# Kernel optimization log

Measured on AMD Instinct MI355X. Metric: run time of the kernel, lower is better.

## Reference

```python
import jax, jax.numpy as jnp
import numpy as np
import math

HID = 2048
NH = 8
KVH = 1
HD = 256
REP = NH // KVH
THETA = 10000.0
B, S = 2, 2048
NEG = -1e9  # additive mask value for disallowed positions


def setup_inputs() -> dict:
    key = jax.random.key(0)
    ks = jax.random.split(key, 6)
    x = jax.random.normal(ks[0], (B, S, HID), dtype=jnp.float32)
    # causal additive mask [B,1,S,S]
    causal = jnp.tril(jnp.ones((S, S), dtype=bool))
    attn_mask = jnp.where(causal, 0.0, NEG).astype(jnp.float32)[None, None]
    attn_mask = jnp.broadcast_to(attn_mask, (B, 1, S, S))
    pos_ids = jnp.broadcast_to(jnp.arange(S, dtype=jnp.int64 if jax.config.jax_enable_x64 else jnp.int32), (B, S))
    sc = 0.02
    wq = jax.random.normal(ks[1], (HID, NH * HD), dtype=jnp.float32) * sc
    wk = jax.random.normal(ks[2], (HID, KVH * HD), dtype=jnp.float32) * sc
    wv = jax.random.normal(ks[3], (HID, KVH * HD), dtype=jnp.float32) * sc
    wo = jax.random.normal(ks[4], (NH * HD, HID), dtype=jnp.float32) * sc
    return {"x": x, "attn_mask": attn_mask, "pos_ids": pos_ids,
            "wq": wq, "wk": wk, "wv": wv, "wo": wo}


def _rotate_half(t):
    h = t.shape[-1] // 2
    return jnp.concatenate([-t[..., h:], t[..., :h]], axis=-1)


def _rope_cos_sin(pos_ids, dtype):
    inv_freq = 1.0 / (THETA ** (jnp.arange(0, HD, 2, dtype=jnp.float32) / HD))  # [HD/2]
    freqs = pos_ids.astype(jnp.float32)[:, :, None] * inv_freq[None, None, :]  # [B,S,HD/2]
    emb = jnp.concatenate([freqs, freqs], axis=-1)                              # [B,S,HD]
    # unsqueeze head dim -> [B,1,S,HD]
    return jnp.cos(emb)[:, None].astype(dtype), jnp.sin(emb)[:, None].astype(dtype)


def reference(x, attn_mask, pos_ids, wq, wk, wv, wo):
    b, s, _ = x.shape
    q = (x @ wq).reshape(b, s, NH, HD).transpose(0, 2, 1, 3)    # [B,NH,S,HD]
    k = (x @ wk).reshape(b, s, KVH, HD).transpose(0, 2, 1, 3)   # [B,KVH,S,HD]
    v = (x @ wv).reshape(b, s, KVH, HD).transpose(0, 2, 1, 3)   # [B,KVH,S,HD]
    cos, sin = _rope_cos_sin(pos_ids, q.dtype)
    q = q * cos + _rotate_half(q) * sin
    k = k * cos + _rotate_half(k) * sin
    # GQA: group query heads over shared KV head instead of materializing repeat_kv
    qg = q.reshape(b, KVH, REP, s, HD)
    scores = jnp.einsum('bgrqd,bgkd->bgrqk', qg, k) / math.sqrt(HD)  # [B,KVH,REP,S,S]
    scores = scores.reshape(b, NH, s, s) + attn_mask
    attn = jax.nn.softmax(scores.astype(jnp.float32), axis=-1).astype(q.dtype)  # [B,NH,S,S]
    # dropout p=0.0 -> identity
    pg = attn.reshape(b, KVH, REP, s, s)
    out = jnp.einsum('bgrqk,bgkd->bgrqd', pg, v).reshape(b, NH, s, HD)
    out = out.transpose(0, 2, 1, 3).reshape(b, s, NH * HD) @ wo  # [B,S,HID]
    return out, attn
```

## Files before the change

### kernel.cpp

```cpp
#include <hip/hip_runtime.h>
#include <cstdint>
#include <cmath>

#define HID_ 2048
#define NH_ 8
#define HD_ 256
#define B_ 2
#define S_ 2048
#define BS_ (B_*S_)
#define QKVW_ 2560

typedef short short8 __attribute__((ext_vector_type(8)));
typedef float floatx4 __attribute__((ext_vector_type(4)));

static __device__ __forceinline__ unsigned short f2bf(float f) {
  union { float f; unsigned u; } v; v.f = f;
  return (unsigned short)((v.u + 0x7FFFu + ((v.u >> 16) & 1u)) >> 16);
}
static __device__ __forceinline__ float bf2f(unsigned short h) {
  union { unsigned u; float f; } v; v.u = ((unsigned)h) << 16;
  return v.f;
}

static __device__ __forceinline__ void gload_lds16(const void* g, void* l) {
  __builtin_amdgcn_global_load_lds(
      (const __attribute__((address_space(1))) unsigned int*)g,
      (__attribute__((address_space(3))) unsigned int*)l, 16, 0, 0);
}


__global__ void cast_f32_bf16_k(const float* __restrict__ in, unsigned short* __restrict__ out, long n) {
  long i = ((long)blockIdx.x * blockDim.x + threadIdx.x) * 4;
  if (i >= n) return;
  float4 v = *reinterpret_cast<const float4*>(in + i);
  ushort4 o; o.x = f2bf(v.x); o.y = f2bf(v.y); o.z = f2bf(v.z); o.w = f2bf(v.w);
  *reinterpret_cast<ushort4*>(out + i) = o;
}

__global__ void transpose_f2b_k(const float* __restrict__ in, unsigned short* __restrict__ out, int R, int C) {
  __shared__ float tile[32][33];
  int c0 = blockIdx.x * 32, r0 = blockIdx.y * 32;
  int tx = threadIdx.x, ty = threadIdx.y;
  #pragma unroll
  for (int i = 0; i < 4; i++)
    tile[ty + i*8][tx] = in[(long)(r0 + ty + i*8) * C + c0 + tx];
  __syncthreads();
  #pragma unroll
  for (int i = 0; i < 4; i++)
    out[(long)(c0 + ty + i*8) * R + r0 + tx] = f2bf(tile[tx][ty + i*8]);
}

__global__ void transpose_strided_k(const unsigned short* __restrict__ in, unsigned short* __restrict__ out,
                                    int ld_in, int ld_out, long in_bs, long out_bs) {
  __shared__ unsigned short tile[32][33];
  in += (long)blockIdx.z * in_bs; out += (long)blockIdx.z * out_bs;
  int c0 = blockIdx.x * 32, r0 = blockIdx.y * 32;
  int tx = threadIdx.x, ty = threadIdx.y;
  #pragma unroll
  for (int i = 0; i < 4; i++)
    tile[ty + i*8][tx] = in[(long)(r0 + ty + i*8) * ld_in + c0 + tx];
  __syncthreads();
  #pragma unroll
  for (int i = 0; i < 4; i++)
    out[(long)(c0 + ty + i*8) * ld_out + r0 + tx] = tile[tx][ty + i*8];
}

__global__ void rope_k(unsigned short* __restrict__ qk, const int* __restrict__ pos_ids,
                       int heads, int row_stride, long total) {
  long idx = (long)blockIdx.x * blockDim.x + threadIdx.x;
  if (idx >= total) return;
  int per_row = heads * (HD_/2);
  int r  = (int)(idx / per_row);
  int rem = (int)(idx % per_row);
  int h = rem / (HD_/2);
  int i = rem % (HD_/2);
  float posf = (float)pos_ids[r];
  float freq = expf(-(float)i * (logf(10000.0f) / 128.0f));
  float ang = posf * freq;
  float c = cosf(ang), s = sinf(ang);
  unsigned short* p = qk + (long)r * row_stride + (long)h * HD_;
  float a = bf2f(p[i]), b = bf2f(p[i + 128]);
  p[i]       = f2bf(a * c - b * s);
  p[i + 128] = f2bf(b * c + a * s);
}

template<int EPI>
__global__ __launch_bounds__(256)
void gemm_bt_k(const void* __restrict__ Av, const unsigned short* __restrict__ Bt,
               void* __restrict__ Cv, int K, long lda, long ldb, long ldc) {
  __shared__ unsigned short Al[128 * 32];
  __shared__ unsigned short Bl[128 * 32];

  int tid = threadIdx.x;
  int lane = tid & 63, wave = tid >> 6;
  int bm = blockIdx.y * 128, bn = blockIdx.x * 128;

  const unsigned short* Abase = (const unsigned short*)Av + (long)bm * lda;
  const unsigned short* Bbase = Bt + (long)bn * ldb;

  floatx4 zero = {0.f, 0.f, 0.f, 0.f};
  floatx4 acc[4][4];
  #pragma unroll
  for (int i = 0; i < 4; i++)
    #pragma unroll
    for (int j = 0; j < 4; j++) acc[i][j] = zero;

  const int wm = (wave >> 1) * 64, wn = (wave & 1) * 64;
  const int lr = lane & 15, lq = lane >> 4;

  for (int k0 = 0; k0 < K; k0 += 32) {
    #pragma unroll
    for (int c = 0; c < 2; c++) {
      int e = c * 2048 + tid * 8;
      int row = e >> 5, col = e & 31;
      gload_lds16(Abase + (long)row * lda + k0 + col, (char*)Al + c * 4096 + wave * 1024);
    }
    #pragma unroll
    for (int c = 0; c < 2; c++) {
      int e = c * 2048 + tid * 8;
      int row = e >> 5, col = e & 31;
      gload_lds16(Bbase + (long)row * ldb + k0 + col, (char*)Bl + c * 4096 + wave * 1024);
    }
    __syncthreads();

    short8 af[4], bfr[4];
    #pragma unroll
    for (int i = 0; i < 4; i++)
      af[i] = *reinterpret_cast<const short8*>(&Al[(wm + i*16 + lr) * 32 + lq * 8]);
    #pragma unroll
    for (int j = 0; j < 4; j++)
      bfr[j] = *reinterpret_cast<const short8*>(&Bl[(wn + j*16 + lr) * 32 + lq * 8]);
    #pragma unroll
    for (int i = 0; i < 4; i++)
      #pragma unroll
      for (int j = 0; j < 4; j++)
        acc[i][j] = __builtin_amdgcn_mfma_f32_16x16x32_bf16(af[i], bfr[j], acc[i][j], 0, 0, 0);
    __syncthreads();
  }

  if (EPI == 0) {
    unsigned short* C = (unsigned short*)Cv;
    #pragma unroll
    for (int i = 0; i < 4; i++)
      #pragma unroll
      for (int r = 0; r < 4; r++) {
        int row = bm + wm + i*16 + lq*4 + r;
        #pragma unroll
        for (int j = 0; j < 4; j++) {
          int col = bn + wn + j*16 + lr;
          C[(long)row * ldc + col] = f2bf(acc[i][j][r]);
        }
      }
  } else {
    float* C = (float*)Cv;
    #pragma unroll
    for (int i = 0; i < 4; i++)
      #pragma unroll
      for (int r = 0; r < 4; r++) {
        int row = bm + wm + i*16 + lq*4 + r;
        #pragma unroll
        for (int j = 0; j < 4; j++) {
          int col = bn + wn + j*16 + lr;
          C[(long)row * ldc + col] = acc[i][j][r];
        }
      }
  }
}

__global__ __launch_bounds__(256, 2)
void attn_fused_k(const unsigned short* __restrict__ qkv, const unsigned short* __restrict__ v_t,
                  float* __restrict__ attn, unsigned short* __restrict__ o_bf,
                  float* __restrict__ rowinv) {
  int z = blockIdx.x;
  int b = z >> 3, h = z & 7;
  int t = 31 - blockIdx.y;
  int bm = t * 64;
  int nkt = t / 2 + 1;

  const unsigned short* Qg = qkv + (long)b * S_ * QKVW_ + (long)h * HD_;
  const unsigned short* Kg = qkv + (long)b * S_ * QKVW_ + 2048;
  const unsigned short* Vt = v_t + (long)b * HD_ * S_;
  float* Az = attn + (long)z * S_ * S_;

  __shared__ unsigned short Ql[64 * 256];
  __shared__ unsigned short KPl[128 * 64];
  __shared__ unsigned short Vl[128 * 64];

  int tid = threadIdx.x;
  int lane = tid & 63, wave = tid >> 6;
  int lr = lane & 15, lq = lane >> 4;
  int lx = lr & 7;

  {
    int ce = nkt * 128;
    int perrow = (S_ - ce) >> 2;
    float4 zf = {0.f, 0.f, 0.f, 0.f};
    for (int i = tid; i < 64 * perrow; i += 256) {
      int r = i / perrow, c = i - r * perrow;
      *reinterpret_cast<float4*>(Az + (long)(bm + r) * S_ + ce + c * 4) = zf;
    }
  }

  #pragma unroll
  for (int c = 0; c < 8; c++) {
    int q = c * 256 + tid;
    int row = q >> 5, g = q & 31;
    gload_lds16(Qg + (long)(bm + row) * QKVW_ + ((g ^ (row & 7)) << 3),
                (char*)Ql + c * 4096 + wave * 1024);
  }

  floatx4 zero = {0.f, 0.f, 0.f, 0.f};
  floatx4 oacc[16];
  #pragma unroll
  for (int j = 0; j < 16; j++) oacc[j] = zero;
  float rsum[4] = {0.f, 0.f, 0.f, 0.f};

  for (int kt = 0; kt < nkt; kt++) {
    floatx4 sacc[8];
    #pragma unroll
    for (int j = 0; j < 8; j++) sacc[j] = zero;

    #pragma unroll
    for (int k0 = 0; k0 < HD_; k0 += 64) {
      #pragma unroll
      for (int c = 0; c < 4; c++) {
        int q = c * 256 + tid;
        int row = q >> 3, g = q & 7;
        gload_lds16(Kg + (long)(kt * 128 + row) * QKVW_ + k0 + ((g ^ (row & 7)) << 3),
                    (char*)KPl + c * 4096 + wave * 1024);
      }
      __syncthreads();
      #pragma unroll
      for (int kk = 0; kk < 2; kk++) {
        int gq = (k0 >> 3) + kk * 4 + lq;
        short8 aq = *reinterpret_cast<const short8*>(&Ql[(wave*16 + lr) * 256 + ((gq ^ lx) << 3)]);
        #pragma unroll
        for (int j = 0; j < 8; j++) {
          short8 bk = *reinterpret_cast<const short8*>(&KPl[(j*16 + lr) * 64 + (((kk*4 + lq) ^ lx) << 3)]);
          sacc[j] = __builtin_amdgcn_mfma_f32_16x16x32_bf16(aq, bk, sacc[j], 0, 0, 0);
        }
      }
      __syncthreads();
    }

    #pragma unroll
    for (int j = 0; j < 8; j++)
      #pragma unroll
      for (int r = 0; r < 4; r++) {
        int row_l = wave*16 + lq*4 + r;
        int col_g = kt*128 + j*16 + lr;
        float p = (col_g <= bm + row_l) ? __expf(sacc[j][r] * 0.0625f) : 0.f;
        Az[(long)(bm + row_l) * S_ + col_g] = p;
        KPl[row_l * 128 + ((j*16 + lr) ^ ((row_l & 7) << 3))] = f2bf(p);
        rsum[r] += p;
      }

    #pragma unroll
    for (int ch = 0; ch < 2; ch++) {
      short8 ap[2];
      #pragma unroll
      for (int kk = 0; kk < 2; kk++)
        ap[kk] = *reinterpret_cast<const short8*>(
            &KPl[(wave*16 + lr) * 128 + ((ch*64 + kk*32 + lq*8) ^ (lx << 3))]);
      #pragma unroll
      for (int dh = 0; dh < 2; dh++) {
        #pragma unroll
        for (int c = 0; c < 4; c++) {
          int q = c * 256 + tid;
          int row = q >> 3, g = q & 7;
          gload_lds16(Vt + (long)(dh*128 + row) * S_ + kt*128 + ch*64 + ((g ^ (row & 7)) << 3),
                      (char*)Vl + c * 4096 + wave * 1024);
        }
        __syncthreads();
        #pragma unroll
        for (int kk = 0; kk < 2; kk++) {
          #pragma unroll
          for (int j2 = 0; j2 < 8; j2++) {
            short8 bv = *reinterpret_cast<const short8*>(
                &Vl[(j2*16 + lr) * 64 + (((kk*4 + lq) ^ lx) << 3)]);
            oacc[dh*8 + j2] = __builtin_amdgcn_mfma_f32_16x16x32_bf16(ap[kk], bv, oacc[dh*8 + j2], 0, 0, 0);
          }
        }
        __syncthreads();
      }
    }
  }

  #pragma unroll
  for (int r = 0; r < 4; r++) {
    float s = rsum[r];
    #pragma unroll
    for (int o = 1; o < 16; o <<= 1) s += __shfl_xor(s, o, 64);
    rsum[r] = 1.0f / s;
  }
  if (lr == 0) {
    #pragma unroll
    for (int r = 0; r < 4; r++)
      rowinv[(long)z * S_ + bm + wave*16 + lq*4 + r] = rsum[r];
  }

  unsigned short* C = o_bf + (long)b * S_ * HID_ + (long)h * HD_;
  #pragma unroll
  for (int dh = 0; dh < 2; dh++)
    #pragma unroll
    for (int j2 = 0; j2 < 8; j2++)
      #pragma unroll
      for (int r = 0; r < 4; r++) {
        int row = bm + wave*16 + lq*4 + r;
        int col = dh*128 + j2*16 + lr;
        C[(long)row * HID_ + col] = f2bf(oacc[dh*8 + j2][r] * rsum[r]);
      }
}

__global__ __launch_bounds__(256)
void attn_rescale_k(float* __restrict__ attn, const float* __restrict__ rowinv) {
  int z = blockIdx.y;
  int i = blockIdx.x;
  int m = (int)((sqrtf(8.f * (float)i + 1.f) - 1.f) * 0.5f);
  while ((m + 1) * (m + 2) / 2 <= i) m++;
  while (m * (m + 1) / 2 > i) m--;
  int n = i - m * (m + 1) / 2;

  int tid = threadIdx.x;
  int rr = tid >> 5, cc = tid & 31;
  float* base = attn + (long)z * S_ * S_ + (long)(m * 128) * S_ + n * 128;
  const float* invb = rowinv + (long)z * S_ + m * 128;
  #pragma unroll 4
  for (int it = 0; it < 16; it++) {
    int row = it * 8 + rr;
    float inv = invb[row];
    float4* p = reinterpret_cast<float4*>(base + (long)row * S_) + cc;
    float4 v = *p;
    v.x *= inv; v.y *= inv; v.z *= inv; v.w *= inv;
    *p = v;
  }
}


extern "C" void kernel_launch(void* const* d_in, const int* in_sizes, int n_in,
                              void* d_out, int out_size, void* d_ws, size_t ws_size,
                              hipStream_t stream) {
  (void)in_sizes; (void)n_in; (void)out_size; (void)ws_size;
  const float* x   = (const float*)d_in[0];
  const int*   pos = (const int*)d_in[2];
  const float* wq  = (const float*)d_in[3];
  const float* wk  = (const float*)d_in[4];
  const float* wv  = (const float*)d_in[5];
  const float* wo  = (const float*)d_in[6];
  float* out  = (float*)d_out;
  float* attn = out + (long)B_ * S_ * HID_;

  char* p = (char*)d_ws;
  auto take = [&](size_t n) { char* r = p; p += (n + 255) & ~(size_t)255; return r; };
  unsigned short* x_bf   = (unsigned short*)take((size_t)BS_ * HID_ * 2);
  unsigned short* wqkv_t = (unsigned short*)take((size_t)QKVW_ * HID_ * 2);
  unsigned short* wo_t   = (unsigned short*)take((size_t)HID_ * HID_ * 2);
  unsigned short* qkv    = (unsigned short*)take((size_t)BS_ * QKVW_ * 2);
  unsigned short* v_t    = (unsigned short*)take((size_t)B_ * HD_ * S_ * 2);
  unsigned short* o_bf   = (unsigned short*)take((size_t)BS_ * HID_ * 2);
  float*          rinv   = (float*)take((size_t)B_ * NH_ * S_ * 4);

  dim3 tb(32, 8);

  cast_f32_bf16_k<<<(BS_ * HID_) / 1024, 256, 0, stream>>>(x, x_bf, (long)BS_ * HID_);

  transpose_f2b_k<<<dim3(HID_/32, HID_/32), tb, 0, stream>>>(wq, wqkv_t, HID_, HID_);
  transpose_f2b_k<<<dim3(HD_/32,  HID_/32), tb, 0, stream>>>(wk, wqkv_t + (size_t)2048 * HID_, HID_, HD_);
  transpose_f2b_k<<<dim3(HD_/32,  HID_/32), tb, 0, stream>>>(wv, wqkv_t + (size_t)2304 * HID_, HID_, HD_);
  transpose_f2b_k<<<dim3(HID_/32, HID_/32), tb, 0, stream>>>(wo, wo_t, HID_, HID_);

  gemm_bt_k<0><<<dim3(QKVW_/128, BS_/128), 256, 0, stream>>>(
      x_bf, wqkv_t, qkv, HID_, HID_, HID_, QKVW_);

  rope_k<<<(BS_ * NH_ * (HD_/2)) / 256, 256, 0, stream>>>(
      qkv, pos, NH_, QKVW_, (long)BS_ * NH_ * (HD_/2));
  rope_k<<<(BS_ * (HD_/2)) / 256, 256, 0, stream>>>(
      qkv + 2048, pos, 1, QKVW_, (long)BS_ * (HD_/2));

  transpose_strided_k<<<dim3(HD_/32, S_/32, B_), tb, 0, stream>>>(
      qkv + 2304, v_t, QKVW_, S_, (long)S_ * QKVW_, (long)HD_ * S_);

  attn_fused_k<<<dim3(B_ * NH_, S_/64), 256, 0, stream>>>(qkv, v_t, attn, o_bf, rinv);

  attn_rescale_k<<<dim3(136, B_ * NH_), 256, 0, stream>>>(attn, rinv);

  gemm_bt_k<1><<<dim3(HID_/128, BS_/128), 256, 0, stream>>>(
      o_bf, wo_t, out, HID_, HID_, HID_, HID_);
}
```

Measured before the change: 694.1 us.

## Double-buffer K/V tiles in LDS and keep Q fragments in registers

Restructures the fused attention loop to double-buffer K and V tiles in shared memory, issuing the next chunk's async loads before computing on the current one so each stage needs only one barrier instead of two. Q is loaded once into registers instead of LDS, which frees shared memory. Attention-probability stores are paired through a lane shuffle into float2 writes. This adds register pressure from the 8 Q fragments and more complex buffer-index logic, and reuses a K buffer to hold P.

```diff
diff --git a/kernel.cpp b/kernel.cpp
--- a/kernel.cpp
+++ b/kernel.cpp
@@ -182,14 +182,12 @@
   const unsigned short* Vt = v_t + (long)b * HD_ * S_;
   float* Az = attn + (long)z * S_ * S_;
 
-  __shared__ unsigned short Ql[64 * 256];
-  __shared__ unsigned short KPl[128 * 64];
-  __shared__ unsigned short Vl[128 * 64];
+  __shared__ unsigned short Kb[2][128 * 64];
+  __shared__ unsigned short Vb[2][128 * 64];
 
   int tid = threadIdx.x;
   int lane = tid & 63, wave = tid >> 6;
   int lr = lane & 15, lq = lane >> 4;
-  int lx = lr & 7;
 
   {
     int ce = nkt * 128;
@@ -201,13 +199,37 @@
     }
   }
 
-  #pragma unroll
-  for (int c = 0; c < 8; c++) {
-    int q = c * 256 + tid;
-    int row = q >> 5, g = q & 31;
-    gload_lds16(Qg + (long)(bm + row) * QKVW_ + ((g ^ (row & 7)) << 3),
-                (char*)Ql + c * 4096 + wave * 1024);
-  }
+  short8 aq[8];
+  {
+    const unsigned short* qrow = Qg + (long)(bm + wave*16 + lr) * QKVW_;
+    #pragma unroll
+    for (int f = 0; f < 8; f++)
+      aq[f] = *reinterpret_cast<const short8*>(qrow + f*32 + lq*8);
+  }
+
+  auto stageK = [&](int kt_, int c_) {
+    char* dst = (char*)Kb[(kt_ + c_) & 1];
+    const unsigned short* src = Kg + (long)(kt_ * 128) * QKVW_ + c_ * 64;
+    #pragma unroll
+    for (int cc = 0; cc < 4; cc++) {
+      int q = cc * 256 + tid;
+      int row = q >> 3, g = q & 7;
+      gload_lds16(src + (long)row * QKVW_ + ((g ^ (row & 7)) << 3),
+                  dst + cc * 4096 + wave * 1024);
+    }
+  };
+  auto stageV = [&](int kt_, int p_) {
+    int dh = p_ & 1, sh = p_ >> 1;
+    char* dst = (char*)Vb[p_ & 1];
+    const unsigned short* src = Vt + (long)(dh * 128) * S_ + kt_ * 128 + sh * 64;
+    #pragma unroll
+    for (int cc = 0; cc < 4; cc++) {
+      int q = cc * 256 + tid;
+      int row = q >> 3, g = q & 7;
+      gload_lds16(src + (long)row * S_ + ((g ^ (row & 7)) << 3),
+                  dst + cc * 4096 + wave * 1024);
+    }
+  };
 
   floatx4 zero = {0.f, 0.f, 0.f, 0.f};
   floatx4 oacc[16];
@@ -215,74 +237,91 @@
   for (int j = 0; j < 16; j++) oacc[j] = zero;
   float rsum[4] = {0.f, 0.f, 0.f, 0.f};
 
+  stageK(0, 0);
+  __syncthreads();
+
   for (int kt = 0; kt < nkt; kt++) {
+    int pb = kt & 1;
     floatx4 sacc[8];
     #pragma unroll
     for (int j = 0; j < 8; j++) sacc[j] = zero;
 
     #pragma unroll
-    for (int k0 = 0; k0 < HD_; k0 += 64) {
-      #pragma unroll
-      for (int c = 0; c < 4; c++) {
-        int q = c * 256 + tid;
-        int row = q >> 3, g = q & 7;
-        gload_lds16(Kg + (long)(kt * 128 + row) * QKVW_ + k0 + ((g ^ (row & 7)) << 3),
-                    (char*)KPl + c * 4096 + wave * 1024);
+    for (int c = 0; c < 4; c++) {
+      if (c < 3) stageK(kt, c + 1);
+      if (c == 2) stageV(kt, 0);
+      if (c == 3) stageV(kt, 1);
+      const unsigned short* Kc = Kb[(kt + c) & 1];
+      #pragma unroll
+      for (int kk = 0; kk < 2; kk++) {
+        #pragma unroll
+        for (int j = 0; j < 8; j++) {
+          int R = j*16 + lr, G = kk*4 + lq;
+          short8 bk = *reinterpret_cast<const short8*>(&Kc[R*64 + ((G ^ (R & 7)) << 3)]);
+          sacc[j] = __builtin_amdgcn_mfma_f32_16x16x32_bf16(aq[c*2 + kk], bk, sacc[j], 0, 0, 0);
+        }
       }
       __syncthreads();
-      #pragma unroll
-      for (int kk = 0; kk < 2; kk++) {
-        int gq = (k0 >> 3) + kk * 4 + lq;
-        short8 aq = *reinterpret_cast<const short8*>(&Ql[(wave*16 + lr) * 256 + ((gq ^ lx) << 3)]);
-        #pragma unroll
-        for (int j = 0; j < 8; j++) {
-          short8 bk = *reinterpret_cast<const short8*>(&KPl[(j*16 + lr) * 64 + (((kk*4 + lq) ^ lx) << 3)]);
-          sacc[j] = __builtin_amdgcn_mfma_f32_16x16x32_bf16(aq, bk, sacc[j], 0, 0, 0);
-        }
-      }
-      __syncthreads();
-    }
-
-    #pragma unroll
-    for (int j = 0; j < 8; j++)
+    }
+
+    unsigned short* Pl = Kb[pb];
+    #pragma unroll
+    for (int j = 0; j < 8; j++) {
+      float v[4];
       #pragma unroll
       for (int r = 0; r < 4; r++) {
         int row_l = wave*16 + lq*4 + r;
         int col_g = kt*128 + j*16 + lr;
-        float p = (col_g <= bm + row_l) ? __expf(sacc[j][r] * 0.0625f) : 0.f;
-        Az[(long)(bm + row_l) * S_ + col_g] = p;
-        KPl[row_l * 128 + ((j*16 + lr) ^ ((row_l & 7) << 3))] = f2bf(p);
-        rsum[r] += p;
-      }
-
-    #pragma unroll
-    for (int ch = 0; ch < 2; ch++) {
+        float pv = (col_g <= bm + row_l) ? __expf(sacc[j][r] * 0.0625f) : 0.f;
+        v[r] = pv;
+        rsum[r] += pv;
+        int Gw = j*2 + (lr >> 3);
+        Pl[row_l*128 + ((Gw ^ (row_l & 7)) << 3) + (lr & 7)] = f2bf(pv);
+      }
+      float w[4];
+      #pragma unroll
+      for (int r = 0; r < 4; r++) w[r] = __shfl_xor(v[r], 1, 64);
+      int colb = kt*128 + j*16 + (lr & ~1);
+      if (!(lr & 1)) {
+        #pragma unroll
+        for (int r = 0; r < 2; r++) {
+          int row = bm + wave*16 + lq*4 + r;
+          float2 st; st.x = v[r]; st.y = w[r];
+          *reinterpret_cast<float2*>(Az + (long)row * S_ + colb) = st;
+        }
+      } else {
+        #pragma unroll
+        for (int r = 2; r < 4; r++) {
+          int row = bm + wave*16 + lq*4 + r;
+          float2 st; st.x = w[r]; st.y = v[r];
+          *reinterpret_cast<float2*>(Az + (long)row * S_ + colb) = st;
+        }
+      }
+    }
+
+    #pragma unroll
+    for (int p = 0; p < 4; p++) {
+      if (p == 0 && kt + 1 < nkt) stageK(kt + 1, 0);
+      if (p == 1) stageV(kt, 2);
+      if (p == 2) stageV(kt, 3);
+      int dh = p & 1, sh = p >> 1;
+      const unsigned short* Vc = Vb[p & 1];
       short8 ap[2];
       #pragma unroll
-      for (int kk = 0; kk < 2; kk++)
-        ap[kk] = *reinterpret_cast<const short8*>(
-            &KPl[(wave*16 + lr) * 128 + ((ch*64 + kk*32 + lq*8) ^ (lx << 3))]);
-      #pragma unroll
-      for (int dh = 0; dh < 2; dh++) {
-        #pragma unroll
-        for (int c = 0; c < 4; c++) {
-          int q = c * 256 + tid;
-          int row = q >> 3, g = q & 7;
-          gload_lds16(Vt + (long)(dh*128 + row) * S_ + kt*128 + ch*64 + ((g ^ (row & 7)) << 3),
-                      (char*)Vl + c * 4096 + wave * 1024);
-        }
-        __syncthreads();
-        #pragma unroll
-        for (int kk = 0; kk < 2; kk++) {
-          #pragma unroll
-          for (int j2 = 0; j2 < 8; j2++) {
-            short8 bv = *reinterpret_cast<const short8*>(
-                &Vl[(j2*16 + lr) * 64 + (((kk*4 + lq) ^ lx) << 3)]);
-            oacc[dh*8 + j2] = __builtin_amdgcn_mfma_f32_16x16x32_bf16(ap[kk], bv, oacc[dh*8 + j2], 0, 0, 0);
-          }
-        }
-        __syncthreads();
-      }
+      for (int kk = 0; kk < 2; kk++) {
+        int R = wave*16 + lr, G = sh*8 + kk*4 + lq;
+        ap[kk] = *reinterpret_cast<const short8*>(&Pl[R*128 + ((G ^ (R & 7)) << 3)]);
+      }
+      #pragma unroll
+      for (int kk = 0; kk < 2; kk++) {
+        #pragma unroll
+        for (int j2 = 0; j2 < 8; j2++) {
+          int R = j2*16 + lr, G = kk*4 + lq;
+          short8 bv = *reinterpret_cast<const short8*>(&Vc[R*64 + ((G ^ (R & 7)) << 3)]);
+          oacc[dh*8 + j2] = __builtin_amdgcn_mfma_f32_16x16x32_bf16(ap[kk], bv, oacc[dh*8 + j2], 0, 0, 0);
+        }
+      }
+      __syncthreads();
     }
   }
 
```

Result: no change. 694.4 us (+0.0%).
